# Kernel optimization log

Measured on AMD Instinct MI355X. Metric: run time of the kernel, lower is better.

The kernel has to match this reference:

```python
import jax, jax.numpy as jnp
import numpy as np

VOCAB, EMB, HID, L = 100000, 128, 256, 9
B, S = 128, 512
H = HID // 2  # per-direction hidden size
PAD = 0


def setup_inputs() -> dict:
    key = jax.random.key(0)
    ks = jax.random.split(key, 18)
    seqs = jax.random.randint(ks[0], (B, S), 1, VOCAB)
    # left-aligned padding: lengths in [S//2, S]
    lens = jax.random.randint(ks[1], (B,), S // 2, S + 1)
    seqs = jnp.where(jnp.arange(S)[None, :] < lens[:, None], seqs, PAD)
    labels = jax.random.randint(ks[2], (B, S), 0, L)

    def n(k, shape, s=0.05):
        return jax.random.normal(k, shape, jnp.float32) * s

    emb = n(ks[3], (VOCAB, EMB)).at[PAD].set(0.0)
    inp = {
        'sequences': seqs, 'labels': labels, 'emb': emb,
        'w_ih_f': n(ks[4], (4 * H, EMB)), 'w_hh_f': n(ks[5], (4 * H, H)),
        'b_ih_f': n(ks[6], (4 * H,)), 'b_hh_f': n(ks[7], (4 * H,)),
        'w_ih_b': n(ks[8], (4 * H, EMB)), 'w_hh_b': n(ks[9], (4 * H, H)),
        'b_ih_b': n(ks[10], (4 * H,)), 'b_hh_b': n(ks[11], (4 * H,)),
        'w_out': n(ks[12], (L, HID)), 'b_out': n(ks[13], (L,)),
        'start_t': n(ks[14], (L,), 0.1), 'end_t': n(ks[15], (L,), 0.1),
        'trans': n(ks[16], (L, L), 0.1),
    }
    return inp


def _lstm_scan(x, w_ih, w_hh, b_ih, b_hh):
    # x: [S, B, E] -> hidden states [S, B, H]
    h0 = jnp.zeros((x.shape[1], w_hh.shape[1]), x.dtype)

    def step(carry, xt):
        h, c = carry
        g = xt @ w_ih.T + b_ih + h @ w_hh.T + b_hh
        i, f, gg, o = jnp.split(g, 4, axis=-1)  # PyTorch gate order i,f,g,o
        c = jax.nn.sigmoid(f) * c + jax.nn.sigmoid(i) * jnp.tanh(gg)
        h = jax.nn.sigmoid(o) * jnp.tanh(c)
        return (h, c), h

    _, hs = jax.lax.scan(step, (h0, h0), x)
    return hs


def reference(sequences, labels, emb, w_ih_f, w_hh_f, b_ih_f, b_hh_f,
              w_ih_b, w_hh_b, b_ih_b, b_hh_b, w_out, b_out,
              start_t, end_t, trans):
    # Embedding lookup (dropout is identity at inference)
    x = emb[sequences]                      # [B,S,E]
    xt = jnp.swapaxes(x, 0, 1)              # [S,B,E]
    hf = _lstm_scan(xt, w_ih_f, w_hh_f, b_ih_f, b_hh_f)
    hb = _lstm_scan(xt[::-1], w_ih_b, w_hh_b, b_ih_b, b_hh_b)[::-1]
    hcat = jnp.concatenate([hf, hb], axis=-1)         # [S,B,HID]
    emissions = jnp.swapaxes(hcat, 0, 1) @ w_out.T + b_out  # [B,S,L]

    mask = sequences != PAD                 # [B,S], first step all True
    maskf = mask.astype(emissions.dtype)

    # --- CRF numerator (score of gold path) ---
    em_tag = jnp.take_along_axis(emissions, labels[..., None], axis=2)[..., 0]  # [B,S]
    trans_sc = trans[labels[:, :-1], labels[:, 1:]]                              # [B,S-1]
    num = start_t[labels[:, 0]] + em_tag[:, 0] \
        + jnp.sum((trans_sc + em_tag[:, 1:]) * maskf[:, 1:], axis=1)
    seq_ends = jnp.sum(mask, axis=1) - 1
    last_tags = labels[jnp.arange(labels.shape[0]), seq_ends]
    num = num + end_t[last_tags]

    # --- CRF partition function (forward algorithm) ---
    def fstep(score, inp):
        em_t, m_t = inp  # [B,L], [B]
        nxt = jax.nn.logsumexp(score[:, :, None] + trans[None] + em_t[:, None, :], axis=1)
        return jnp.where(m_t[:, None], nxt, score), None

    score0 = start_t[None, :] + emissions[:, 0]  # [B,L]
    em_rest = jnp.swapaxes(emissions, 0, 1)[1:]  # [S-1,B,L]
    scoreT, _ = jax.lax.scan(fstep, score0, (em_rest, mask.T[1:]))
    denom = jax.nn.logsumexp(scoreT + end_t[None, :], axis=1)  # [B]

    # model returns -log_likelihood (torchcrf default reduction='sum')
    return -jnp.sum(num - denom)
```

## Files before the change

### kernel.cpp

```cpp
#include <hip/hip_runtime.h>
#include <hip/hip_bf16.h>

#define B_   128
#define S_   512
#define H_   128
#define G_   512
#define EMB_ 128
#define NL_  9

typedef __attribute__((ext_vector_type(8))) short bf16x8;
typedef __attribute__((ext_vector_type(4))) short bf16x4;
typedef __attribute__((ext_vector_type(4))) float f32x4;
typedef unsigned short ushort_t;

__device__ __forceinline__ void wg_bar() {
    asm volatile("s_waitcnt lgkmcnt(0)\n\ts_barrier" ::: "memory");
}

__device__ __forceinline__ float bfbits2f(short s) {
    unsigned int u = ((unsigned int)(unsigned short)s) << 16;
    return __builtin_bit_cast(float, u);
}
__device__ __forceinline__ short f2bf(float f) {
    unsigned int u = __builtin_bit_cast(unsigned int, f);
    u += 0x7FFFu + ((u >> 16) & 1u);
    return (short)(u >> 16);
}
__device__ __forceinline__ unsigned int pack2(float lo, float hi) {
    return (unsigned int)(unsigned short)f2bf(lo) | ((unsigned int)(unsigned short)f2bf(hi) << 16);
}
__device__ __forceinline__ float exp2_(float x) {
    float r; asm("v_exp_f32 %0, %1" : "=v"(r) : "v"(x)); return r;
}
__device__ __forceinline__ float log2_(float x) {
    float r; asm("v_log_f32 %0, %1" : "=v"(r) : "v"(x)); return r;
}
__device__ __forceinline__ float max3_(float a, float b, float c) {
    float r; asm("v_max3_f32 %0, %1, %2, %3" : "=v"(r) : "v"(a), "v"(b), "v"(c)); return r;
}
__device__ __forceinline__ float tanh_(float x) {
    return 1.f - 2.f * __builtin_amdgcn_rcpf(1.f + exp2_(2.8853900817779268f * x));
}

__global__ __launch_bounds__(256)
void prep2_kernel(const float* __restrict__ w_ih_f, const float* __restrict__ w_ih_b,
                  const float* __restrict__ b_ih_f, const float* __restrict__ b_hh_f,
                  const float* __restrict__ b_ih_b, const float* __restrict__ b_hh_b,
                  ushort_t* __restrict__ wihPack, float* __restrict__ biasPack)
{
    const int bid = blockIdx.x, tid = threadIdx.x;
    if (bid < 64) {
        int f = bid * 256 + tid;
        int lane = f & 63;
        int nt  = (f >> 6) & 3;
        int ks  = (f >> 8) & 3;
        int wv8 = (f >> 10) & 7;
        int dirq = (f >> 13) & 1;
        int n16 = lane & 15, quad = lane >> 4;
        const float* w = dirq ? w_ih_b : w_ih_f;
        int col = nt * 128 + wv8 * 16 + n16;
        const float* p = w + col * EMB_ + ks * 32 + quad * 8;
        bf16x8 r;
#pragma unroll
        for (int j = 0; j < 8; j++) r[j] = f2bf(p[j]);
        size_t addr = ((size_t)dirq * 8192 + wv8 * 1024 + ks * 256 + nt * 64 + lane) * 8;
        *(bf16x8*)(wihPack + addr) = r;
    } else {
        int idx = (bid - 64) * 256 + tid;
        if (idx < 1024) {
            int nt  = idx & 3;
            int n16 = (idx >> 2) & 15;
            int wv8 = (idx >> 6) & 7;
            int dirq = (idx >> 9) & 1;
            const float* bi = dirq ? b_ih_b : b_ih_f;
            const float* bh = dirq ? b_hh_b : b_hh_f;
            int col = nt * 128 + wv8 * 16 + n16;
            biasPack[idx] = bi[col] + bh[col];
        }
    }
}

__global__ __launch_bounds__(512, 1)
void xw2_kernel(const int* __restrict__ seq, const float* __restrict__ emb,
                const ushort_t* __restrict__ wihPack, const float* __restrict__ biasPack,
                ushort_t* __restrict__ xw)
{
    __shared__ bf16x8 ldsX[64 * 17];

    const int tid  = threadIdx.x;
    const int wv   = tid >> 6;
    const int lane = tid & 63;
    const int n16  = tid & 15;
    const int quad = (tid & 63) >> 4;
    const int dir  = blockIdx.x >> 10;
    const int rem  = blockIdx.x & 1023;
    const int pair = rem >> 4;
    const int tb   = (rem & 15) * 32;

    {
        int row = tid >> 3, part = tid & 7;
        int b = 2 * pair + (row >> 5);
        int t = tb + (row & 31);
        int tok = seq[b * S_ + t];
        const float* ep = emb + (size_t)tok * EMB_ + part * 16;
        int rt = row >> 4, rr = row & 15;
#pragma unroll
        for (int h = 0; h < 2; h++) {
            float4 a = *(const float4*)(ep + h * 8);
            float4 b4 = *(const float4*)(ep + h * 8 + 4);
            bf16x8 fr;
            fr[0] = f2bf(a.x); fr[1] = f2bf(a.y); fr[2] = f2bf(a.z); fr[3] = f2bf(a.w);
            fr[4] = f2bf(b4.x); fr[5] = f2bf(b4.y); fr[6] = f2bf(b4.z); fr[7] = f2bf(b4.w);
            ldsX[(rt * 16 + part * 2 + h) * 17 + rr] = fr;
        }
    }

    bf16x8 bfrag[4][4];
    float  bias[4];
    {
        const ushort_t* wb = wihPack + ((size_t)dir * 8192 + (size_t)wv * 1024 + lane) * 8;
#pragma unroll
        for (int nt = 0; nt < 4; nt++) {
            bias[nt] = biasPack[((dir * 8 + wv) * 16 + n16) * 4 + nt];
#pragma unroll
            for (int ks = 0; ks < 4; ks++)
                bfrag[nt][ks] = *(const bf16x8*)(wb + (ks * 256 + nt * 64) * 8);
        }
    }
    __syncthreads();

    const size_t plane0 = (size_t)(dir * 128 + 2 * pair);

#pragma unroll
    for (int half = 0; half < 2; half++) {
        f32x4 accA[4], accB[4];
        bf16x8 afA[4], afB[4];
#pragma unroll
        for (int ks = 0; ks < 4; ks++) {
            afA[ks] = ldsX[(half * 16 + ks * 4 + quad) * 17 + n16];
            afB[ks] = ldsX[((half + 2) * 16 + ks * 4 + quad) * 17 + n16];
        }
#pragma unroll
        for (int nt = 0; nt < 4; nt++) {
            f32x4 a = {bias[nt], bias[nt], bias[nt], bias[nt]};
            accA[nt] = a; accB[nt] = a;
#pragma unroll
            for (int ks = 0; ks < 4; ks++) {
                accA[nt] = __builtin_amdgcn_mfma_f32_16x16x32_bf16(afA[ks], bfrag[nt][ks], accA[nt], 0, 0, 0);
                accB[nt] = __builtin_amdgcn_mfma_f32_16x16x32_bf16(afB[ks], bfrag[nt][ks], accB[nt], 0, 0, 0);
            }
        }
        const int u = wv * 16 + n16;
#pragma unroll
        for (int r = 0; r < 4; r++) {
            int t = tb + half * 16 + quad * 4 + r;
            int2 iv0, iv1;
            iv0.x = (int)pack2(accA[0][r], accA[1][r]);
            iv0.y = (int)pack2(accA[2][r], accA[3][r]);
            iv1.x = (int)pack2(accB[0][r], accB[1][r]);
            iv1.y = (int)pack2(accB[2][r], accB[3][r]);
            *(int2*)(xw + ((plane0 * S_ + t) * 128 + u) * 4) = iv0;
            *(int2*)(xw + (((plane0 + 1) * S_ + t) * 128 + u) * 4) = iv1;
        }
    }
}

#define STEPK(k)                                                                   \
  {                                                                                \
    if ((k) == 0 && s4 == 0 && m < 31) {                                           \
      const ushort_t* gp = xwp + (size_t)(dir ? (S_ - 32 - m16) : (m16 + 16)) * 512; \
      sA = *(const int4*)(gp + tid * 8);                                           \
      sB = *(const int4*)(gp + 2048 + tid * 8);                                    \
      sC = *(const int4*)(gp + 4096 + tid * 8);                                    \
      sD = *(const int4*)(gp + 6144 + tid * 8);                                    \
    }                                                                              \
    bf16x8 af0 = hbuf[(k) & 1][0 * 4 + quad];                                      \
    bf16x8 af1 = hbuf[(k) & 1][1 * 4 + quad];                                      \
    bf16x8 af2 = hbuf[(k) & 1][2 * 4 + quad];                                      \
    bf16x8 af3 = hbuf[(k) & 1][3 * 4 + quad];                                      \
    const int KE = s4x4 + (k);                                                     \
    const int slot = dir ? (15 - KE) : KE;                                         \
    bf16x4 xvg = *(const bf16x4*)(xwS + (m & 1) * 8192 + slot * 512 + uu * 4);     \
    if ((k) == 0 && s4 == 2 && m < 31) {                                           \
      int4* dst = (int4*)(xwL + (((m & 1) ^ 1) * 1024));                           \
      dst[tid] = sA; dst[256 + tid] = sB; dst[512 + tid] = sC; dst[768 + tid] = sD; \
    }                                                                              \
    if ((k) == 1 && s4 == 0 && m >= 1 && wv == 3 && lane < 36) {                   \
      int a0 = dir ? (S_ - m16) : (m16 - 16);                                      \
      float4 fv = *(const float4*)(emL + (a0 & 31) * 9 + lane * 4);                \
      *(float4*)(emdir + (size_t)b * (S_ * NL_) + a0 * NL_ + lane * 4) = fv;       \
    }                                                                              \
    f32x4 aA0 = __builtin_amdgcn_mfma_f32_16x16x32_bf16(af0, bfrag[0][0][0], ZACC, 0, 0, 0); \
    f32x4 aA1 = __builtin_amdgcn_mfma_f32_16x16x32_bf16(af0, bfrag[0][1][0], ZACC, 0, 0, 0); \
    f32x4 aA2 = __builtin_amdgcn_mfma_f32_16x16x32_bf16(af0, bfrag[0][2][0], ZACC, 0, 0, 0); \
    f32x4 aA3 = __builtin_amdgcn_mfma_f32_16x16x32_bf16(af0, bfrag[0][3][0], ZACC, 0, 0, 0); \
    f32x4 aB0 = __builtin_amdgcn_mfma_f32_16x16x32_bf16(af0, bfrag[1][0][0], ZACC, 0, 0, 0); \
    f32x4 aB1 = __builtin_amdgcn_mfma_f32_16x16x32_bf16(af0, bfrag[1][1][0], ZACC, 0, 0, 0); \
    f32x4 aB2 = __builtin_amdgcn_mfma_f32_16x16x32_bf16(af0, bfrag[1][2][0], ZACC, 0, 0, 0); \
    f32x4 aB3 = __builtin_amdgcn_mfma_f32_16x16x32_bf16(af0, bfrag[1][3][0], ZACC, 0, 0, 0); \
    aA0 = __builtin_amdgcn_mfma_f32_16x16x32_bf16(af1, bfrag[0][0][1], aA0, 0, 0, 0); \
    aA1 = __builtin_amdgcn_mfma_f32_16x16x32_bf16(af1, bfrag[0][1][1], aA1, 0, 0, 0); \
    aA2 = __builtin_amdgcn_mfma_f32_16x16x32_bf16(af1, bfrag[0][2][1], aA2, 0, 0, 0); \
    aA3 = __builtin_amdgcn_mfma_f32_16x16x32_bf16(af1, bfrag[0][3][1], aA3, 0, 0, 0); \
    aB0 = __builtin_amdgcn_mfma_f32_16x16x32_bf16(af1, bfrag[1][0][1], aB0, 0, 0, 0); \
    aB1 = __builtin_amdgcn_mfma_f32_16x16x32_bf16(af1, bfrag[1][1][1], aB1, 0, 0, 0); \
    aB2 = __builtin_amdgcn_mfma_f32_16x16x32_bf16(af1, bfrag[1][2][1], aB2, 0, 0, 0); \
    aB3 = __builtin_amdgcn_mfma_f32_16x16x32_bf16(af1, bfrag[1][3][1], aB3, 0, 0, 0); \
    aA0 = __builtin_amdgcn_mfma_f32_16x16x32_bf16(af2, bfrag[0][0][2], aA0, 0, 0, 0); \
    aA1 = __builtin_amdgcn_mfma_f32_16x16x32_bf16(af2, bfrag[0][1][2], aA1, 0, 0, 0); \
    aA2 = __builtin_amdgcn_mfma_f32_16x16x32_bf16(af2, bfrag[0][2][2], aA2, 0, 0, 0); \
    aA3 = __builtin_amdgcn_mfma_f32_16x16x32_bf16(af2, bfrag[0][3][2], aA3, 0, 0, 0); \
    aB0 = __builtin_amdgcn_mfma_f32_16x16x32_bf16(af2, bfrag[1][0][2], aB0, 0, 0, 0); \
    aB1 = __builtin_amdgcn_mfma_f32_16x16x32_bf16(af2, bfrag[1][1][2], aB1, 0, 0, 0); \
    aB2 = __builtin_amdgcn_mfma_f32_16x16x32_bf16(af2, bfrag[1][2][2], aB2, 0, 0, 0); \
    aB3 = __builtin_amdgcn_mfma_f32_16x16x32_bf16(af2, bfrag[1][3][2], aB3, 0, 0, 0); \
    aA0 = __builtin_amdgcn_mfma_f32_16x16x32_bf16(af3, bfrag[0][0][3], aA0, 0, 0, 0); \
    aA1 = __builtin_amdgcn_mfma_f32_16x16x32_bf16(af3, bfrag[0][1][3], aA1, 0, 0, 0); \
    aA2 = __builtin_amdgcn_mfma_f32_16x16x32_bf16(af3, bfrag[0][2][3], aA2, 0, 0, 0); \
    aA3 = __builtin_amdgcn_mfma_f32_16x16x32_bf16(af3, bfrag[0][3][3], aA3, 0, 0, 0); \
    aB0 = __builtin_amdgcn_mfma_f32_16x16x32_bf16(af3, bfrag[1][0][3], aB0, 0, 0, 0); \
    aB1 = __builtin_amdgcn_mfma_f32_16x16x32_bf16(af3, bfrag[1][1][3], aB1, 0, 0, 0); \
    aB2 = __builtin_amdgcn_mfma_f32_16x16x32_bf16(af3, bfrag[1][2][3], aB2, 0, 0, 0); \
    aB3 = __builtin_amdgcn_mfma_f32_16x16x32_bf16(af3, bfrag[1][3][3], aB3, 0, 0, 0); \
    {                                                                              \
      float gi = ((quad & 2) ? aB0[0] : aA0[0]) + bfbits2f(xvg[0]);                \
      float gf = ((quad & 2) ? aB1[0] : aA1[0]) + bfbits2f(xvg[1]);                \
      float gg = ((quad & 2) ? aB2[0] : aA2[0]) + bfbits2f(xvg[2]);                \
      float go = ((quad & 2) ? aB3[0] : aA3[0]) + bfbits2f(xvg[3]);                \
      float Af = exp2_(-1.4426950408889634f * gf);                                 \
      float Bi = exp2_(-1.4426950408889634f * gi);                                 \
      float Cg = exp2_(2.8853900817779268f * gg);                                  \
      float Fo = exp2_(-1.4426950408889634f * go);                                 \
      float oA = 1.f + Af, oB = 1.f + Bi, oC = 1.f + Cg;                           \
      float P = oB * oC;                                                           \
      float numer = cst * P + oA * (Cg - 1.f);                                     \
      cst = numer * __builtin_amdgcn_rcpf(oA * P);                                 \
      float hv = tanh_(cst) * __builtin_amdgcn_rcpf(1.f + Fo);                     \
      if (!(quad & 1)) *(((k) & 1) ? hw0 : hw1) = f2bf(hv);                        \
    }                                                                              \
    if (wv == 0) {                                                                 \
      f32x4 accE = __builtin_amdgcn_mfma_f32_16x16x32_bf16(af0, bfragE[0], ZACC, 0, 0, 0); \
      accE = __builtin_amdgcn_mfma_f32_16x16x32_bf16(af1, bfragE[1], accE, 0, 0, 0); \
      accE = __builtin_amdgcn_mfma_f32_16x16x32_bf16(af2, bfragE[2], accE, 0, 0, 0); \
      accE = __builtin_amdgcn_mfma_f32_16x16x32_bf16(af3, bfragE[3], accE, 0, 0, 0); \
      if (quad == 0 && n16 < NL_ && (m16 + KE) >= 1) {                             \
        int tprev = dir ? (S_ - (m16 + KE)) : (m16 + KE - 1);                      \
        emL[(tprev & 31) * 9 + n16] = accE[0];                                     \
      }                                                                            \
    }                                                                              \
    wg_bar();                                                                      \
  }

__global__ __launch_bounds__(256, 1)
void lstm_kernel(const ushort_t* __restrict__ xw,
                 const float* __restrict__ w_hh_f, const float* __restrict__ w_hh_b,
                 const float* __restrict__ w_out,
                 float* __restrict__ em_f, float* __restrict__ em_b)
{
    __shared__ bf16x8 xwL[2 * 1024];
    __shared__ bf16x8 hbuf[2][16];
    __shared__ __align__(16) float emL[32 * NL_];

    const int tid  = threadIdx.x;
    const int wv   = tid >> 6;
    const int lane = tid & 63;
    const int n16  = tid & 15;
    const int quad = (tid & 63) >> 4;
    const int dir  = blockIdx.x >> 7;
    const int b    = blockIdx.x & 127;

    const int uu = wv * 32 + ((quad >> 1) << 4) + n16;

    short* hw0 = ((short*)hbuf) + uu;
    short* hw1 = ((short*)hbuf) + 128 + uu;
    const short* xwS = (const short*)xwL;

    const f32x4 ZACC = {0.f, 0.f, 0.f, 0.f};

    const float* whh = dir ? w_hh_b : w_hh_f;
    float* emdir = dir ? em_b : em_f;

    bf16x8 bfrag[2][4][4];
#pragma unroll
    for (int tl = 0; tl < 2; tl++) {
#pragma unroll
        for (int nt = 0; nt < 4; nt++) {
            int col = nt * 128 + wv * 32 + tl * 16 + n16;
#pragma unroll
            for (int ks = 0; ks < 4; ks++) {
                const float* p = whh + col * H_ + ks * 32 + quad * 8;
                bf16x8 fr;
#pragma unroll
                for (int j = 0; j < 8; j++) fr[j] = f2bf(p[j]);
                bfrag[tl][nt][ks] = fr;
            }
        }
    }
    bf16x8 bfragE[4];
#pragma unroll
    for (int ks = 0; ks < 4; ks++) {
        bf16x8 fr = {0, 0, 0, 0, 0, 0, 0, 0};
        if (n16 < NL_) {
            const float* p = w_out + n16 * 256 + dir * 128 + ks * 32 + quad * 8;
#pragma unroll
            for (int j = 0; j < 8; j++) fr[j] = f2bf(p[j]);
        }
        bfragE[ks] = fr;
    }

    if (tid < 64) ((int*)hbuf)[tid] = 0;

    const ushort_t* xwp = xw + (size_t)(dir * 128 + b) * ((size_t)S_ * 512);
    {
        const ushort_t* gp = xwp + (size_t)(dir ? (S_ - 16) : 0) * 512;
        int4 a0 = *(const int4*)(gp + tid * 8);
        int4 a1 = *(const int4*)(gp + 2048 + tid * 8);
        int4 a2 = *(const int4*)(gp + 4096 + tid * 8);
        int4 a3 = *(const int4*)(gp + 6144 + tid * 8);
        int4* dst = (int4*)xwL;
        dst[tid] = a0; dst[256 + tid] = a1; dst[512 + tid] = a2; dst[768 + tid] = a3;
    }

    float cst = 0.f;
    int4 sA, sB, sC, sD;
    wg_bar();

#pragma unroll 1
    for (int m = 0; m < 32; m++) {
        const int m16 = m << 4;
#pragma unroll 1
        for (int s4 = 0; s4 < 4; s4++) {
            const int s4x4 = s4 << 2;
            STEPK(0) STEPK(1) STEPK(2) STEPK(3)
        }
    }

    if (wv == 0) {
        bf16x8 af0 = hbuf[0][0 * 4 + quad];
        bf16x8 af1 = hbuf[0][1 * 4 + quad];
        bf16x8 af2 = hbuf[0][2 * 4 + quad];
        bf16x8 af3 = hbuf[0][3 * 4 + quad];
        f32x4 accE = __builtin_amdgcn_mfma_f32_16x16x32_bf16(af0, bfragE[0], ZACC, 0, 0, 0);
        accE = __builtin_amdgcn_mfma_f32_16x16x32_bf16(af1, bfragE[1], accE, 0, 0, 0);
        accE = __builtin_amdgcn_mfma_f32_16x16x32_bf16(af2, bfragE[2], accE, 0, 0, 0);
        accE = __builtin_amdgcn_mfma_f32_16x16x32_bf16(af3, bfragE[3], accE, 0, 0, 0);
        if (quad == 0 && n16 < NL_) {
            int tprev = dir ? 0 : (S_ - 1);
            emL[(tprev & 31) * 9 + n16] = accE[0];
        }
    }
    wg_bar();
    if (wv == 3 && lane < 36) {
        int a0 = dir ? 0 : (S_ - 16);
        float4 fv = *(const float4*)(emL + (a0 & 31) * 9 + lane * 4);
        *(float4*)(emdir + (size_t)b * (S_ * NL_) + a0 * NL_ + lane * 4) = fv;
    }
}

__global__ __launch_bounds__(640, 1)
void crf_kernel(const int* __restrict__ seq, const int* __restrict__ lab,
                const float* __restrict__ em_f, const float* __restrict__ em_b,
                const float* __restrict__ b_out,
                const float* __restrict__ start_t, const float* __restrict__ end_t,
                const float* __restrict__ trans, float* __restrict__ partial)
{
    __shared__ float emS[S_ * NL_];
    __shared__ float transS[NL_ * NL_];
    __shared__ float stS[NL_], enS[NL_];
    __shared__ unsigned char maskS[S_];
    __shared__ float MS[7 * 81];
    __shared__ float vS[NL_];
    __shared__ float redw[10];
    __shared__ int   redl[10];

    const int b = blockIdx.x, tid = threadIdx.x;
    const size_t base = (size_t)b * S_ * NL_;
    const float L2E = 1.4426950408889634f, LN2 = 0.6931471805599453f;

    for (int q = tid; q < S_ * NL_; q += 640)
        emS[q] = em_f[base + q] + em_b[base + q] + b_out[q % NL_];
    if (tid < NL_ * NL_) transS[tid] = trans[tid];
    if (tid < NL_) { stS[tid] = start_t[tid]; enS[tid] = end_t[tid]; }
    if (tid < S_) maskS[tid] = (seq[b * S_ + tid] != 0);
    __syncthreads();

    float np = 0.f; int myc = 0;
    if (tid < S_) {
        myc = maskS[tid];
        if (tid >= 1 && maskS[tid]) {
            int lp = lab[b * S_ + tid - 1], lc = lab[b * S_ + tid];
            np = transS[lp * NL_ + lc] + emS[tid * NL_ + lc];
        }
    }
#pragma unroll
    for (int off = 32; off; off >>= 1) {
        np  += __shfl_down(np, off, 64);
        myc += __shfl_down(myc, off, 64);
    }
    if ((tid & 63) == 0) { redw[tid >> 6] = np; redl[tid >> 6] = myc; }

    const int w = tid >> 6, l = tid & 63;
    const int lg = l / 9;
    const int g  = w * 7 + lg;
    const bool sact = (lg < 7) && (g < 64);
    const int jj = sact ? (l - lg * 9) : 0;
    const int gb = sact ? lg * 9 : 0;
    float Tc[NL_];
#pragma unroll
    for (int i = 0; i < NL_; i++) Tc[i] = transS[i * NL_ + jj];
    float sc; int tbeg, tend, cN = 0, iN = 0;
    if (sact && g == 0) {
        sc = stS[jj] + emS[jj];
        tbeg = 1; tend = 64;
    } else if (sact) {
        cN = 1 + (g - 1) / 9; iN = (g - 1) % 9;
        sc = (jj == iN) ? 0.f : -1e30f;
        tbeg = cN * 64; tend = tbeg + 64;
    } else {
        sc = -1e30f; tbeg = 448; tend = 512;
    }
    for (int t = tbeg; t < tend; t++) {
        float emv = emS[t * NL_ + jj];
        float a[NL_];
#pragma unroll
        for (int i = 0; i < NL_; i++) a[i] = __shfl(sc, gb + i, 64) + Tc[i];
        float m = max3_(max3_(a[0], a[1], a[2]), max3_(a[3], a[4], a[5]),
                        max3_(a[6], a[7], a[8]));
        float e[NL_];
#pragma unroll
        for (int i = 0; i < NL_; i++) e[i] = exp2_((a[i] - m) * L2E);
        float sum = ((e[0] + e[1]) + (e[2] + e[3])) + ((e[4] + e[5]) + (e[6] + e[7])) + e[8];
        float nxt = emv + m + LN2 * log2_(sum);
        sc = maskS[t] ? nxt : sc;
    }
    if (sact) {
        if (g == 0) vS[jj] = sc;
        else MS[(cN - 1) * 81 + iN * NL_ + jj] = sc;
    }
    __syncthreads();

    if (tid < 64) {
        const int j = (tid < NL_) ? tid : (NL_ - 1);
        float v = vS[j];
        for (int c = 1; c < 8; c++) {
            float a[NL_];
#pragma unroll
            for (int i = 0; i < NL_; i++)
                a[i] = __shfl(v, i, 64) + MS[(c - 1) * 81 + i * NL_ + j];
            float m = max3_(max3_(a[0], a[1], a[2]), max3_(a[3], a[4], a[5]),
                            max3_(a[6], a[7], a[8]));
            float e[NL_];
#pragma unroll
            for (int i = 0; i < NL_; i++) e[i] = exp2_((a[i] - m) * L2E);
            float sum = ((e[0] + e[1]) + (e[2] + e[3])) + ((e[4] + e[5]) + (e[6] + e[7])) + e[8];
            v = m + LN2 * log2_(sum);
        }
        v += enS[j];
        float mm = -1e30f, av[NL_];
#pragma unroll
        for (int i = 0; i < NL_; i++) { float vi = __shfl(v, i, 64); av[i] = vi; mm = fmaxf(mm, vi); }
        float ss = 0.f;
#pragma unroll
        for (int i = 0; i < NL_; i++) ss += exp2_((av[i] - mm) * L2E);
        if (tid == 0) {
            float num = 0.f; int len = 0;
#pragma unroll
            for (int ww = 0; ww < 10; ww++) { num += redw[ww]; len += redl[ww]; }
            int l0 = lab[b * S_];
            int ll = lab[b * S_ + len - 1];
            num += stS[l0] + emS[l0] + enS[ll];
            partial[b] = (mm + LN2 * log2_(ss)) - num;
        }
    }
}

__global__ __launch_bounds__(128)
void reduce_kernel(const float* __restrict__ partial, float* __restrict__ out)
{
    __shared__ float s[128];
    int tid = threadIdx.x;
    s[tid] = partial[tid];
    __syncthreads();
    for (int off = 64; off; off >>= 1) {
        if (tid < off) s[tid] += s[tid + off];
        __syncthreads();
    }
    if (tid == 0) out[0] = s[0];
}

extern "C" void kernel_launch(void* const* d_in, const int* in_sizes, int n_in,
                              void* d_out, int out_size, void* d_ws, size_t ws_size,
                              hipStream_t stream)
{
    const int* seq = (const int*)d_in[0];
    const int* lab = (const int*)d_in[1];
    const float* emb    = (const float*)d_in[2];
    const float* w_ih_f = (const float*)d_in[3];
    const float* w_hh_f = (const float*)d_in[4];
    const float* b_ih_f = (const float*)d_in[5];
    const float* b_hh_f = (const float*)d_in[6];
    const float* w_ih_b = (const float*)d_in[7];
    const float* w_hh_b = (const float*)d_in[8];
    const float* b_ih_b = (const float*)d_in[9];
    const float* b_hh_b = (const float*)d_in[10];
    const float* w_out  = (const float*)d_in[11];
    const float* b_out  = (const float*)d_in[12];
    const float* start_t = (const float*)d_in[13];
    const float* end_t   = (const float*)d_in[14];
    const float* trans   = (const float*)d_in[15];

    char* ws = (char*)d_ws;
    const size_t xw_bytes   = (size_t)2 * B_ * S_ * G_ * sizeof(ushort_t);
    const size_t wih_bytes  = (size_t)16384 * 16;
    const size_t bias_bytes = 1024 * sizeof(float);
    const size_t em_bytes   = (size_t)B_ * S_ * NL_ * sizeof(float);

    ushort_t* xw      = (ushort_t*)ws;
    ushort_t* wihPack = (ushort_t*)(ws + xw_bytes);
    float* biasPack   = (float*)(ws + xw_bytes + wih_bytes);
    float* em_f       = (float*)(ws + xw_bytes + wih_bytes + bias_bytes);
    float* em_b       = (float*)(ws + xw_bytes + wih_bytes + bias_bytes + em_bytes);
    float* partial    = (float*)(ws + xw_bytes + wih_bytes + bias_bytes + 2 * em_bytes);

    prep2_kernel<<<dim3(68), dim3(256), 0, stream>>>(w_ih_f, w_ih_b,
        b_ih_f, b_hh_f, b_ih_b, b_hh_b, wihPack, biasPack);
    xw2_kernel<<<dim3(2048), dim3(512), 0, stream>>>(seq, emb, wihPack, biasPack, xw);
    lstm_kernel<<<dim3(256), dim3(256), 0, stream>>>(xw, w_hh_f, w_hh_b,
        w_out, em_f, em_b);
    crf_kernel<<<dim3(B_), dim3(640), 0, stream>>>(seq, lab, em_f, em_b, b_out,
        start_t, end_t, trans, partial);
    reduce_kernel<<<dim3(1), dim3(128), 0, stream>>>(partial, (float*)d_out);
}
```

Measured before the change: 441.5 us.

## Double LSTM recurrent block to 8 waves, halving MFMAs per wave

The recurrent LSTM kernel now runs 512 threads (8 waves) per block instead of 256, so each wave owns 16 hidden units rather than 32. That halves the per-step MFMA chain and the register-resident W_hh fragments per wave, and the xw prefetch is split across twice as many threads. The aim is a shorter critical path per serial timestep, at the cost of more waves taking part in every per-step barrier and redundant gate math, since only quad 0 writes h.

```diff
diff --git a/kernel.cpp b/kernel.cpp
--- a/kernel.cpp
+++ b/kernel.cpp
@@ -170,9 +170,7 @@
     if ((k) == 0 && s4 == 0 && m < 31) {                                           \
       const ushort_t* gp = xwp + (size_t)(dir ? (S_ - 32 - m16) : (m16 + 16)) * 512; \
       sA = *(const int4*)(gp + tid * 8);                                           \
-      sB = *(const int4*)(gp + 2048 + tid * 8);                                    \
-      sC = *(const int4*)(gp + 4096 + tid * 8);                                    \
-      sD = *(const int4*)(gp + 6144 + tid * 8);                                    \
+      sB = *(const int4*)(gp + 4096 + tid * 8);                                    \
     }                                                                              \
     bf16x8 af0 = hbuf[(k) & 1][0 * 4 + quad];                                      \
     bf16x8 af1 = hbuf[(k) & 1][1 * 4 + quad];                                      \
@@ -183,50 +181,34 @@
     bf16x4 xvg = *(const bf16x4*)(xwS + (m & 1) * 8192 + slot * 512 + uu * 4);     \
     if ((k) == 0 && s4 == 2 && m < 31) {                                           \
       int4* dst = (int4*)(xwL + (((m & 1) ^ 1) * 1024));                           \
-      dst[tid] = sA; dst[256 + tid] = sB; dst[512 + tid] = sC; dst[768 + tid] = sD; \
+      dst[tid] = sA; dst[512 + tid] = sB;                                          \
     }                                                                              \
-    if ((k) == 1 && s4 == 0 && m >= 1 && wv == 3 && lane < 36) {                   \
+    if ((k) == 1 && s4 == 0 && m >= 1 && wv == 7 && lane < 36) {                   \
       int a0 = dir ? (S_ - m16) : (m16 - 16);                                      \
       float4 fv = *(const float4*)(emL + (a0 & 31) * 9 + lane * 4);                \
       *(float4*)(emdir + (size_t)b * (S_ * NL_) + a0 * NL_ + lane * 4) = fv;       \
     }                                                                              \
-    f32x4 aA0 = __builtin_amdgcn_mfma_f32_16x16x32_bf16(af0, bfrag[0][0][0], ZACC, 0, 0, 0); \
-    f32x4 aA1 = __builtin_amdgcn_mfma_f32_16x16x32_bf16(af0, bfrag[0][1][0], ZACC, 0, 0, 0); \
-    f32x4 aA2 = __builtin_amdgcn_mfma_f32_16x16x32_bf16(af0, bfrag[0][2][0], ZACC, 0, 0, 0); \
-    f32x4 aA3 = __builtin_amdgcn_mfma_f32_16x16x32_bf16(af0, bfrag[0][3][0], ZACC, 0, 0, 0); \
-    f32x4 aB0 = __builtin_amdgcn_mfma_f32_16x16x32_bf16(af0, bfrag[1][0][0], ZACC, 0, 0, 0); \
-    f32x4 aB1 = __builtin_amdgcn_mfma_f32_16x16x32_bf16(af0, bfrag[1][1][0], ZACC, 0, 0, 0); \
-    f32x4 aB2 = __builtin_amdgcn_mfma_f32_16x16x32_bf16(af0, bfrag[1][2][0], ZACC, 0, 0, 0); \
-    f32x4 aB3 = __builtin_amdgcn_mfma_f32_16x16x32_bf16(af0, bfrag[1][3][0], ZACC, 0, 0, 0); \
-    aA0 = __builtin_amdgcn_mfma_f32_16x16x32_bf16(af1, bfrag[0][0][1], aA0, 0, 0, 0); \
-    aA1 = __builtin_amdgcn_mfma_f32_16x16x32_bf16(af1, bfrag[0][1][1], aA1, 0, 0, 0); \
-    aA2 = __builtin_amdgcn_mfma_f32_16x16x32_bf16(af1, bfrag[0][2][1], aA2, 0, 0, 0); \
-    aA3 = __builtin_amdgcn_mfma_f32_16x16x32_bf16(af1, bfrag[0][3][1], aA3, 0, 0, 0); \
-    aB0 = __builtin_amdgcn_mfma_f32_16x16x32_bf16(af1, bfrag[1][0][1], aB0, 0, 0, 0); \
-    aB1 = __builtin_amdgcn_mfma_f32_16x16x32_bf16(af1, bfrag[1][1][1], aB1, 0, 0, 0); \
-    aB2 = __builtin_amdgcn_mfma_f32_16x16x32_bf16(af1, bfrag[1][2][1], aB2, 0, 0, 0); \
-    aB3 = __builtin_amdgcn_mfma_f32_16x16x32_bf16(af1, bfrag[1][3][1], aB3, 0, 0, 0); \
-    aA0 = __builtin_amdgcn_mfma_f32_16x16x32_bf16(af2, bfrag[0][0][2], aA0, 0, 0, 0); \
-    aA1 = __builtin_amdgcn_mfma_f32_16x16x32_bf16(af2, bfrag[0][1][2], aA1, 0, 0, 0); \
-    aA2 = __builtin_amdgcn_mfma_f32_16x16x32_bf16(af2, bfrag[0][2][2], aA2, 0, 0, 0); \
-    aA3 = __builtin_amdgcn_mfma_f32_16x16x32_bf16(af2, bfrag[0][3][2], aA3, 0, 0, 0); \
-    aB0 = __builtin_amdgcn_mfma_f32_16x16x32_bf16(af2, bfrag[1][0][2], aB0, 0, 0, 0); \
-    aB1 = __builtin_amdgcn_mfma_f32_16x16x32_bf16(af2, bfrag[1][1][2], aB1, 0, 0, 0); \
-    aB2 = __builtin_amdgcn_mfma_f32_16x16x32_bf16(af2, bfrag[1][2][2], aB2, 0, 0, 0); \
-    aB3 = __builtin_amdgcn_mfma_f32_16x16x32_bf16(af2, bfrag[1][3][2], aB3, 0, 0, 0); \
-    aA0 = __builtin_amdgcn_mfma_f32_16x16x32_bf16(af3, bfrag[0][0][3], aA0, 0, 0, 0); \
-    aA1 = __builtin_amdgcn_mfma_f32_16x16x32_bf16(af3, bfrag[0][1][3], aA1, 0, 0, 0); \
-    aA2 = __builtin_amdgcn_mfma_f32_16x16x32_bf16(af3, bfrag[0][2][3], aA2, 0, 0, 0); \
-    aA3 = __builtin_amdgcn_mfma_f32_16x16x32_bf16(af3, bfrag[0][3][3], aA3, 0, 0, 0); \
-    aB0 = __builtin_amdgcn_mfma_f32_16x16x32_bf16(af3, bfrag[1][0][3], aB0, 0, 0, 0); \
-    aB1 = __builtin_amdgcn_mfma_f32_16x16x32_bf16(af3, bfrag[1][1][3], aB1, 0, 0, 0); \
-    aB2 = __builtin_amdgcn_mfma_f32_16x16x32_bf16(af3, bfrag[1][2][3], aB2, 0, 0, 0); \
-    aB3 = __builtin_amdgcn_mfma_f32_16x16x32_bf16(af3, bfrag[1][3][3], aB3, 0, 0, 0); \
+    f32x4 aA0 = __builtin_amdgcn_mfma_f32_16x16x32_bf16(af0, bfrag[0][0], ZACC, 0, 0, 0); \
+    f32x4 aA1 = __builtin_amdgcn_mfma_f32_16x16x32_bf16(af0, bfrag[1][0], ZACC, 0, 0, 0); \
+    f32x4 aA2 = __builtin_amdgcn_mfma_f32_16x16x32_bf16(af0, bfrag[2][0], ZACC, 0, 0, 0); \
+    f32x4 aA3 = __builtin_amdgcn_mfma_f32_16x16x32_bf16(af0, bfrag[3][0], ZACC, 0, 0, 0); \
+    aA0 = __builtin_amdgcn_mfma_f32_16x16x32_bf16(af1, bfrag[0][1], aA0, 0, 0, 0); \
+    aA1 = __builtin_amdgcn_mfma_f32_16x16x32_bf16(af1, bfrag[1][1], aA1, 0, 0, 0); \
+    aA2 = __builtin_amdgcn_mfma_f32_16x16x32_bf16(af1, bfrag[2][1], aA2, 0, 0, 0); \
+    aA3 = __builtin_amdgcn_mfma_f32_16x16x32_bf16(af1, bfrag[3][1], aA3, 0, 0, 0); \
+    aA0 = __builtin_amdgcn_mfma_f32_16x16x32_bf16(af2, bfrag[0][2], aA0, 0, 0, 0); \
+    aA1 = __builtin_amdgcn_mfma_f32_16x16x32_bf16(af2, bfrag[1][2], aA1, 0, 0, 0); \
+    aA2 = __builtin_amdgcn_mfma_f32_16x16x32_bf16(af2, bfrag[2][2], aA2, 0, 0, 0); \
+    aA3 = __builtin_amdgcn_mfma_f32_16x16x32_bf16(af2, bfrag[3][2], aA3, 0, 0, 0); \
+    aA0 = __builtin_amdgcn_mfma_f32_16x16x32_bf16(af3, bfrag[0][3], aA0, 0, 0, 0); \
+    aA1 = __builtin_amdgcn_mfma_f32_16x16x32_bf16(af3, bfrag[1][3], aA1, 0, 0, 0); \
+    aA2 = __builtin_amdgcn_mfma_f32_16x16x32_bf16(af3, bfrag[2][3], aA2, 0, 0, 0); \
+    aA3 = __builtin_amdgcn_mfma_f32_16x16x32_bf16(af3, bfrag[3][3], aA3, 0, 0, 0); \
     {                                                                              \
-      float gi = ((quad & 2) ? aB0[0] : aA0[0]) + bfbits2f(xvg[0]);                \
-      float gf = ((quad & 2) ? aB1[0] : aA1[0]) + bfbits2f(xvg[1]);                \
-      float gg = ((quad & 2) ? aB2[0] : aA2[0]) + bfbits2f(xvg[2]);                \
-      float go = ((quad & 2) ? aB3[0] : aA3[0]) + bfbits2f(xvg[3]);                \
+      float gi = aA0[0] + bfbits2f(xvg[0]);                                        \
+      float gf = aA1[0] + bfbits2f(xvg[1]);                                        \
+      float gg = aA2[0] + bfbits2f(xvg[2]);                                        \
+      float go = aA3[0] + bfbits2f(xvg[3]);                                        \
       float Af = exp2_(-1.4426950408889634f * gf);                                 \
       float Bi = exp2_(-1.4426950408889634f * gi);                                 \
       float Cg = exp2_(2.8853900817779268f * gg);                                  \
@@ -236,7 +218,7 @@
       float numer = cst * P + oA * (Cg - 1.f);                                     \
       cst = numer * __builtin_amdgcn_rcpf(oA * P);                                 \
       float hv = tanh_(cst) * __builtin_amdgcn_rcpf(1.f + Fo);                     \
-      if (!(quad & 1)) *(((k) & 1) ? hw0 : hw1) = f2bf(hv);                        \
+      if (quad == 0) *(((k) & 1) ? hw0 : hw1) = f2bf(hv);                          \
     }                                                                              \
     if (wv == 0) {                                                                 \
       f32x4 accE = __builtin_amdgcn_mfma_f32_16x16x32_bf16(af0, bfragE[0], ZACC, 0, 0, 0); \
@@ -251,7 +233,7 @@
     wg_bar();                                                                      \
   }
 
-__global__ __launch_bounds__(256, 1)
+__global__ __launch_bounds__(512, 1)
 void lstm_kernel(const ushort_t* __restrict__ xw,
                  const float* __restrict__ w_hh_f, const float* __restrict__ w_hh_b,
                  const float* __restrict__ w_out,
@@ -269,7 +251,7 @@
     const int dir  = blockIdx.x >> 7;
     const int b    = blockIdx.x & 127;
 
-    const int uu = wv * 32 + ((quad >> 1) << 4) + n16;
+    const int uu = wv * 16 + n16;
 
     short* hw0 = ((short*)hbuf) + uu;
     short* hw1 = ((short*)hbuf) + 128 + uu;
@@ -280,20 +262,17 @@
     const float* whh = dir ? w_hh_b : w_hh_f;
     float* emdir = dir ? em_b : em_f;
 
-    bf16x8 bfrag[2][4][4];
-#pragma unroll
-    for (int tl = 0; tl < 2; tl++) {
-#pragma unroll
-        for (int nt = 0; nt < 4; nt++) {
-            int col = nt * 128 + wv * 32 + tl * 16 + n16;
-#pragma unroll
-            for (int ks = 0; ks < 4; ks++) {
-                const float* p = whh + col * H_ + ks * 32 + quad * 8;
-                bf16x8 fr;
-#pragma unroll
-                for (int j = 0; j < 8; j++) fr[j] = f2bf(p[j]);
-                bfrag[tl][nt][ks] = fr;
-            }
+    bf16x8 bfrag[4][4];
+#pragma unroll
+    for (int nt = 0; nt < 4; nt++) {
+        int col = nt * 128 + wv * 16 + n16;
+#pragma unroll
+        for (int ks = 0; ks < 4; ks++) {
+            const float* p = whh + col * H_ + ks * 32 + quad * 8;
+            bf16x8 fr;
+#pragma unroll
+            for (int j = 0; j < 8; j++) fr[j] = f2bf(p[j]);
+            bfrag[nt][ks] = fr;
         }
     }
     bf16x8 bfragE[4];
@@ -314,15 +293,13 @@
     {
         const ushort_t* gp = xwp + (size_t)(dir ? (S_ - 16) : 0) * 512;
         int4 a0 = *(const int4*)(gp + tid * 8);
-        int4 a1 = *(const int4*)(gp + 2048 + tid * 8);
-        int4 a2 = *(const int4*)(gp + 4096 + tid * 8);
-        int4 a3 = *(const int4*)(gp + 6144 + tid * 8);
+        int4 a1 = *(const int4*)(gp + 4096 + tid * 8);
         int4* dst = (int4*)xwL;
-        dst[tid] = a0; dst[256 + tid] = a1; dst[512 + tid] = a2; dst[768 + tid] = a3;
+        dst[tid] = a0; dst[512 + tid] = a1;
     }
 
     float cst = 0.f;
-    int4 sA, sB, sC, sD;
+    int4 sA, sB;
     wg_bar();
 
 #pragma unroll 1
@@ -350,7 +327,7 @@
         }
     }
     wg_bar();
-    if (wv == 3 && lane < 36) {
+    if (wv == 7 && lane < 36) {
         int a0 = dir ? 0 : (S_ - 16);
         float4 fv = *(const float4*)(emL + (a0 & 31) * 9 + lane * 4);
         *(float4*)(emdir + (size_t)b * (S_ * NL_) + a0 * NL_ + lane * 4) = fv;
@@ -525,7 +502,7 @@
     prep2_kernel<<<dim3(68), dim3(256), 0, stream>>>(w_ih_f, w_ih_b,
         b_ih_f, b_hh_f, b_ih_b, b_hh_b, wihPack, biasPack);
     xw2_kernel<<<dim3(2048), dim3(512), 0, stream>>>(seq, emb, wihPack, biasPack, xw);
-    lstm_kernel<<<dim3(256), dim3(256), 0, stream>>>(xw, w_hh_f, w_hh_b,
+    lstm_kernel<<<dim3(256), dim3(512), 0, stream>>>(xw, w_hh_f, w_hh_b,
         w_out, em_f, em_b);
     crf_kernel<<<dim3(B_), dim3(640), 0, stream>>>(seq, lab, em_f, em_b, b_out,
         start_t, end_t, trans, partial);
```

Measured after the change: 433.8 us. Within noise of the previous version (-1.8%).
